# Kernel optimization log

Measured on AMD Instinct MI355X. Metric: run time of the kernel, lower is better.

The kernel has to match this reference:

```python
import jax, jax.numpy as jnp
import numpy as np

KERNEL = 3  # 2*half_size + 1 with half_size=1
ITER = 20


def _pool(v):
    # MaxPool2d(kernel=3, stride=1, padding=1) == SAME max reduce_window on NCHW
    return jax.lax.reduce_window(v, -jnp.inf, jax.lax.max,
                                 (1, 1, KERNEL, KERNEL), (1, 1, 1, 1), 'SAME')


def _erode(v):
    return -_pool(-v)


def setup_inputs() -> dict:
    key = jax.random.key(0)
    x = jax.random.normal(key, (16, 1, 1024, 1024), dtype=jnp.float32)
    return {"x": x}


def reference(x):
    skel0 = x - _pool(_erode(x))  # open(x) = dilate(erode(x))

    def step(carry, _):
        xc, skel = carry
        xc = _erode(xc)
        skel = skel + (xc - _pool(_erode(xc)))
        return (xc, skel), None

    (_, skel), _ = jax.lax.scan(step, (x, skel0), None, length=ITER)
    return skel
```

## Files before the change

kernel.cpp:

```cpp
#include <hip/hip_runtime.h>


static constexpr int W = 1024, H = 1024, NIMG = 16;
static constexpr int RCH = 32;
static constexpr int NSTEP = RCH + 16;
static constexpr int WPB = 4;
static constexpr float BIG = 3.0e38f;

__device__ __forceinline__ float min3f(float a, float b, float c) { return fminf(fminf(a, b), c); }
__device__ __forceinline__ float max3f(float a, float b, float c) { return fmaxf(fmaxf(a, b), c); }

__device__ __forceinline__ float dpp_left(float v) {
    return __int_as_float(__builtin_amdgcn_mov_dpp(__float_as_int(v), 0x138, 0xF, 0xF, true));
}
__device__ __forceinline__ float dpp_right(float v) {
    return __int_as_float(__builtin_amdgcn_mov_dpp(__float_as_int(v), 0x130, 0xF, 0xF, true));
}

template<bool FIRST, bool WRITE_E, bool EDGE, bool LE, bool RE, int SOFF>
__device__ __forceinline__
void pipe_step(int t, int y0, int gx,
               bool leftEdge, bool rightEdge, bool lane_ok,
               const float* __restrict__ in, float* __restrict__ eo,
               float* __restrict__ sk,
               float4 (&OB)[7], float4 (&MB)[7], float4& OD, float4& MD,
               float4 (&acc)[8], float4 (&pf)[2], float4 (&skpf)[2])
{
    constexpr int PFI = SOFF;

    float4 cur;
    if (!EDGE || (unsigned)t < (unsigned)H) cur = pf[PFI];
    else                                    cur = make_float4(BIG, BIG, BIG, BIG);
    {
        const int nr = t + 2;
        if ((!EDGE || (unsigned)nr < (unsigned)H) && nr <= y0 + RCH + 7)
            pf[PFI] = *(const float4*)&in[(size_t)nr * W + gx];
    }

#pragma unroll
    for (int s = 0; s < 7; ++s) {
        const float4 fOld = OB[s];
        const float4 fMid = MB[s];

        float4 vm;
        vm.x = min3f(fOld.x, fMid.x, cur.x);
        vm.y = min3f(fOld.y, fMid.y, cur.y);
        vm.z = min3f(fOld.z, fMid.z, cur.z);
        vm.w = min3f(fOld.w, fMid.w, cur.w);
        float lft = dpp_left(vm.w);
        float rgt = dpp_right(vm.x);
        if (LE && leftEdge)  lft = BIG;
        if (RE && rightEdge) rgt = BIG;
        float4 en;
        en.x = min3f(lft,  vm.x, vm.y);
        en.y = min3f(vm.x, vm.y, vm.z);
        en.z = min3f(vm.y, vm.z, vm.w);
        en.w = min3f(vm.z, vm.w, rgt);

        OB[s] = cur;

        float4 gOld, gMid;
        if (s < 6) { gOld = OB[s + 1]; gMid = MB[s + 1]; }
        else       { gOld = OD;        gMid = MD;        }
        const bool topOK = !EDGE || ((t - s - 3) >= 0);
        const bool botOK = !EDGE || ((t - s - 1) < H);
        float4 vx;
        {
            float txx = topOK ? gOld.x : -BIG, bxx = botOK ? en.x : -BIG;
            float txy = topOK ? gOld.y : -BIG, bxy = botOK ? en.y : -BIG;
            float txz = topOK ? gOld.z : -BIG, bxz = botOK ? en.z : -BIG;
            float txw = topOK ? gOld.w : -BIG, bxw = botOK ? en.w : -BIG;
            vx.x = max3f(txx, gMid.x, bxx);
            vx.y = max3f(txy, gMid.y, bxy);
            vx.z = max3f(txz, gMid.z, bxz);
            vx.w = max3f(txw, gMid.w, bxw);
        }
        float dl = dpp_left(vx.w);
        float dr = dpp_right(vx.x);
        if (LE && leftEdge)  dl = -BIG;
        if (RE && rightEdge) dr = -BIG;
        float4 dn;
        dn.x = max3f(dl,   vx.x, vx.y);
        dn.y = max3f(vx.x, vx.y, vx.z);
        dn.z = max3f(vx.y, vx.z, vx.w);
        dn.w = max3f(vx.z, vx.w, dr);

        constexpr int base = SOFF + 6;
        const int slot = base - s;
        if (s == 0) {
            acc[slot].x = fOld.x - dn.x;
            acc[slot].y = fOld.y - dn.y;
            acc[slot].z = fOld.z - dn.z;
            acc[slot].w = fOld.w - dn.w;
        } else {
            acc[slot].x += fOld.x - dn.x;
            acc[slot].y += fOld.y - dn.y;
            acc[slot].z += fOld.z - dn.z;
            acc[slot].w += fOld.w - dn.w;
        }

        if (s == 6) {
            if (WRITE_E) {
                const int er = t - 7;
                if (er >= y0 && er < y0 + RCH && lane_ok)
                    *(float4*)&eo[(size_t)er * W + gx] = en;
            }
            OD = en;
        }
        cur = en;
    }

    if (t >= y0 + 8) {
        const int r = t - 8;
        float4 v = acc[SOFF];
        if (!FIRST) {
            const float4 o = skpf[PFI];
            v.x += o.x; v.y += o.y; v.z += o.z; v.w += o.w;
        }
        if (lane_ok)
            *(float4*)&sk[(size_t)r * W + gx] = v;
    }

    if (!FIRST) {
        const int pr = t - 6;
        if (pr >= y0 && pr < y0 + RCH)
            skpf[PFI] = *(const float4*)&sk[(size_t)pr * W + gx];
    }
}

template<bool FIRST, bool WRITE_E, bool EDGE, bool LE, bool RE>
__device__ __forceinline__
void sweep(int y0, int gx,
           bool leftEdge, bool rightEdge, bool lane_ok,
           const float* __restrict__ in, float* __restrict__ eo,
           float* __restrict__ sk)
{
    float4 B0[7], B1[7], D0, D1, acc[8], pf[2], skpf[2];
    const float4 big4 = make_float4(BIG, BIG, BIG, BIG);
    const float4 z4   = make_float4(0.f, 0.f, 0.f, 0.f);
#pragma unroll
    for (int s = 0; s < 7; ++s) { B0[s] = big4; B1[s] = big4; }
    D0 = big4; D1 = big4;
#pragma unroll
    for (int j = 0; j < 8; ++j) acc[j] = z4;
    pf[0] = big4; pf[1] = big4; skpf[0] = z4; skpf[1] = z4;

    {
        const int r0 = y0 - 8, r1 = y0 - 7;
        if (!EDGE || r0 >= 0) pf[0] = *(const float4*)&in[(size_t)r0 * W + gx];
        if (!EDGE || r1 >= 0) pf[1] = *(const float4*)&in[(size_t)r1 * W + gx];
    }

    const int t0 = y0 - 8;
#pragma unroll 1
    for (int t = t0; t < t0 + NSTEP; t += 2) {
        pipe_step<FIRST, WRITE_E, EDGE, LE, RE, 0>(t,     y0, gx, leftEdge, rightEdge, lane_ok,
                                                   in, eo, sk, B0, B1, D0, D1, acc, pf, skpf);
        pipe_step<FIRST, WRITE_E, EDGE, LE, RE, 1>(t + 1, y0, gx, leftEdge, rightEdge, lane_ok,
                                                   in, eo, sk, B1, B0, D1, D0, acc, pf, skpf);
#pragma unroll
        for (int j = 0; j < 6; ++j) acc[j] = acc[j + 2];
    }
}

template<bool FIRST, bool WRITE_E>
__global__ __launch_bounds__(WPB * 64)
void skel_pipe(const float* __restrict__ ein, float* __restrict__ eout,
               float* __restrict__ skel)
{
    const int lane = threadIdx.x;
    const int bx = blockIdx.x;
    const int y0 = (blockIdx.y * WPB + (int)threadIdx.y) * RCH;
    const int img = blockIdx.z;
    const int x0 = (bx == 4) ? 768 : bx * 240;
    const int gx = x0 + 4 * lane;

    const size_t base = (size_t)img * (size_t)(W * H);
    const float* __restrict__ in = ein + base;
    float* __restrict__ eo = eout + base;
    float* __restrict__ sk = skel + base;

    const bool leftEdge  = (gx == 0);
    const bool rightEdge = (gx + 4 == W);
    const int own_lo = (bx == 0) ? 0 : ((bx == 4) ? 968 : x0 + 8);
    const int own_hi = (bx == 4) ? W : x0 + 248;
    const bool lane_ok = (gx >= own_lo) && (gx < own_hi);

    const bool edge_chunk = !(y0 >= 32 && y0 <= H - RCH - 32);

    if (bx == 0) {
        if (edge_chunk) sweep<FIRST, WRITE_E, true,  true,  false>(y0, gx, leftEdge, rightEdge, lane_ok, in, eo, sk);
        else            sweep<FIRST, WRITE_E, false, true,  false>(y0, gx, leftEdge, rightEdge, lane_ok, in, eo, sk);
    } else if (bx == 4) {
        if (edge_chunk) sweep<FIRST, WRITE_E, true,  false, true >(y0, gx, leftEdge, rightEdge, lane_ok, in, eo, sk);
        else            sweep<FIRST, WRITE_E, false, false, true >(y0, gx, leftEdge, rightEdge, lane_ok, in, eo, sk);
    } else {
        if (edge_chunk) sweep<FIRST, WRITE_E, true,  false, false>(y0, gx, leftEdge, rightEdge, lane_ok, in, eo, sk);
        else            sweep<FIRST, WRITE_E, false, false, false>(y0, gx, leftEdge, rightEdge, lane_ok, in, eo, sk);
    }
}

extern "C" void kernel_launch(void* const* d_in, const int* in_sizes, int n_in,
                              void* d_out, int out_size, void* d_ws, size_t ws_size,
                              hipStream_t stream)
{
    const float* x = (const float*)d_in[0];
    float* skel = (float*)d_out;
    const size_t n = (size_t)NIMG * W * H;

    float* e0 = (float*)d_ws;
    float* e1 = e0 + n;

    dim3 grid(5, H / (RCH * WPB), NIMG);
    dim3 block(64, WPB);

    skel_pipe<true,  true ><<<grid, block, 0, stream>>>(x,  e0, skel);
    skel_pipe<false, true ><<<grid, block, 0, stream>>>(e0, e1, skel);
    skel_pipe<false, false><<<grid, block, 0, stream>>>(e1, e0, skel);
}
```

Measured before the change: 337.2 us.

## Process two rows per pipeline step sharing vertical min/max windows

Merges the two per-row pipeline steps into one step that computes a pair of output rows together, sharing the middle-row loads between both vertical 3-tap min/max windows. This cuts redundant register moves and recomputation across the seven erosion/opening stages. It also seeds the accumulators with the prior skeleton values, loaded ahead of time, instead of keeping a separate prefetch buffer, and drops the edge-mask selects on interior chunks. The trade-off is more live registers per step, which may lower occupancy or cause spills.

```diff
diff --git a/kernel.cpp b/kernel.cpp
--- a/kernel.cpp
+++ b/kernel.cpp
@@ -17,24 +17,26 @@
     return __int_as_float(__builtin_amdgcn_mov_dpp(__float_as_int(v), 0x130, 0xF, 0xF, true));
 }
 
-template<bool FIRST, bool WRITE_E, bool EDGE, bool LE, bool RE, int SOFF>
+template<bool FIRST, bool WRITE_E, bool EDGE, bool LE, bool RE>
 __device__ __forceinline__
-void pipe_step(int t, int y0, int gx,
-               bool leftEdge, bool rightEdge, bool lane_ok,
-               const float* __restrict__ in, float* __restrict__ eo,
-               float* __restrict__ sk,
-               float4 (&OB)[7], float4 (&MB)[7], float4& OD, float4& MD,
-               float4 (&acc)[8], float4 (&pf)[2], float4 (&skpf)[2])
-{
-    constexpr int PFI = SOFF;
-
-    float4 cur;
-    if (!EDGE || (unsigned)t < (unsigned)H) cur = pf[PFI];
-    else                                    cur = make_float4(BIG, BIG, BIG, BIG);
+void pipe_step2(int t, int y0, int gx,
+                bool leftEdge, bool rightEdge, bool lane_ok,
+                const float* __restrict__ in, float* __restrict__ eo,
+                float* __restrict__ sk,
+                float4 (&OB)[7], float4 (&MB)[7], float4& OD, float4& MD,
+                float4 (&acc)[8], float4 (&pf)[2])
+{
+    float4 cur0, cur1;
+    if (!EDGE || (unsigned)t < (unsigned)H)       cur0 = pf[0];
+    else                                          cur0 = make_float4(BIG, BIG, BIG, BIG);
+    if (!EDGE || (unsigned)(t + 1) < (unsigned)H) cur1 = pf[1];
+    else                                          cur1 = make_float4(BIG, BIG, BIG, BIG);
     {
-        const int nr = t + 2;
-        if ((!EDGE || (unsigned)nr < (unsigned)H) && nr <= y0 + RCH + 7)
-            pf[PFI] = *(const float4*)&in[(size_t)nr * W + gx];
+        const int n0 = t + 2, n1 = t + 3;
+        if ((!EDGE || (unsigned)n0 < (unsigned)H) && n0 <= y0 + RCH + 7)
+            pf[0] = *(const float4*)&in[(size_t)n0 * W + gx];
+        if ((!EDGE || (unsigned)n1 < (unsigned)H) && n1 <= y0 + RCH + 7)
+            pf[1] = *(const float4*)&in[(size_t)n1 * W + gx];
     }
 
 #pragma unroll
@@ -42,89 +44,111 @@
         const float4 fOld = OB[s];
         const float4 fMid = MB[s];
 
-        float4 vm;
-        vm.x = min3f(fOld.x, fMid.x, cur.x);
-        vm.y = min3f(fOld.y, fMid.y, cur.y);
-        vm.z = min3f(fOld.z, fMid.z, cur.z);
-        vm.w = min3f(fOld.w, fMid.w, cur.w);
-        float lft = dpp_left(vm.w);
-        float rgt = dpp_right(vm.x);
-        if (LE && leftEdge)  lft = BIG;
-        if (RE && rightEdge) rgt = BIG;
-        float4 en;
-        en.x = min3f(lft,  vm.x, vm.y);
-        en.y = min3f(vm.x, vm.y, vm.z);
-        en.z = min3f(vm.y, vm.z, vm.w);
-        en.w = min3f(vm.z, vm.w, rgt);
-
-        OB[s] = cur;
+        float4 vm0, vm1;
+        vm0.x = min3f(fOld.x, fMid.x, cur0.x);
+        vm0.y = min3f(fOld.y, fMid.y, cur0.y);
+        vm0.z = min3f(fOld.z, fMid.z, cur0.z);
+        vm0.w = min3f(fOld.w, fMid.w, cur0.w);
+        vm1.x = min3f(fMid.x, cur0.x, cur1.x);
+        vm1.y = min3f(fMid.y, cur0.y, cur1.y);
+        vm1.z = min3f(fMid.z, cur0.z, cur1.z);
+        vm1.w = min3f(fMid.w, cur0.w, cur1.w);
+        float l0 = dpp_left(vm0.w), r0 = dpp_right(vm0.x);
+        float l1 = dpp_left(vm1.w), r1 = dpp_right(vm1.x);
+        if (LE && leftEdge)  { l0 = BIG; l1 = BIG; }
+        if (RE && rightEdge) { r0 = BIG; r1 = BIG; }
+        float4 en0, en1;
+        en0.x = min3f(l0,    vm0.x, vm0.y);
+        en0.y = min3f(vm0.x, vm0.y, vm0.z);
+        en0.z = min3f(vm0.y, vm0.z, vm0.w);
+        en0.w = min3f(vm0.z, vm0.w, r0);
+        en1.x = min3f(l1,    vm1.x, vm1.y);
+        en1.y = min3f(vm1.x, vm1.y, vm1.z);
+        en1.z = min3f(vm1.y, vm1.z, vm1.w);
+        en1.w = min3f(vm1.z, vm1.w, r1);
 
         float4 gOld, gMid;
         if (s < 6) { gOld = OB[s + 1]; gMid = MB[s + 1]; }
         else       { gOld = OD;        gMid = MD;        }
-        const bool topOK = !EDGE || ((t - s - 3) >= 0);
-        const bool botOK = !EDGE || ((t - s - 1) < H);
-        float4 vx;
-        {
-            float txx = topOK ? gOld.x : -BIG, bxx = botOK ? en.x : -BIG;
-            float txy = topOK ? gOld.y : -BIG, bxy = botOK ? en.y : -BIG;
-            float txz = topOK ? gOld.z : -BIG, bxz = botOK ? en.z : -BIG;
-            float txw = topOK ? gOld.w : -BIG, bxw = botOK ? en.w : -BIG;
-            vx.x = max3f(txx, gMid.x, bxx);
-            vx.y = max3f(txy, gMid.y, bxy);
-            vx.z = max3f(txz, gMid.z, bxz);
-            vx.w = max3f(txw, gMid.w, bxw);
-        }
-        float dl = dpp_left(vx.w);
-        float dr = dpp_right(vx.x);
-        if (LE && leftEdge)  dl = -BIG;
-        if (RE && rightEdge) dr = -BIG;
-        float4 dn;
-        dn.x = max3f(dl,   vx.x, vx.y);
-        dn.y = max3f(vx.x, vx.y, vx.z);
-        dn.z = max3f(vx.y, vx.z, vx.w);
-        dn.w = max3f(vx.z, vx.w, dr);
-
-        constexpr int base = SOFF + 6;
-        const int slot = base - s;
-        if (s == 0) {
-            acc[slot].x = fOld.x - dn.x;
-            acc[slot].y = fOld.y - dn.y;
-            acc[slot].z = fOld.z - dn.z;
-            acc[slot].w = fOld.w - dn.w;
+        float4 vx0, vx1;
+        if (!EDGE) {
+            vx0.x = max3f(gOld.x, gMid.x, en0.x);
+            vx0.y = max3f(gOld.y, gMid.y, en0.y);
+            vx0.z = max3f(gOld.z, gMid.z, en0.z);
+            vx0.w = max3f(gOld.w, gMid.w, en0.w);
+            vx1.x = max3f(gMid.x, en0.x, en1.x);
+            vx1.y = max3f(gMid.y, en0.y, en1.y);
+            vx1.z = max3f(gMid.z, en0.z, en1.z);
+            vx1.w = max3f(gMid.w, en0.w, en1.w);
         } else {
-            acc[slot].x += fOld.x - dn.x;
-            acc[slot].y += fOld.y - dn.y;
-            acc[slot].z += fOld.z - dn.z;
-            acc[slot].w += fOld.w - dn.w;
-        }
+            const bool topOK0 = (t - s - 3) >= 0, botOK0 = (t - s - 1) < H;
+            const bool topOK1 = (t - s - 2) >= 0, botOK1 = (t - s) < H;
+            vx0.x = max3f(topOK0 ? gOld.x : -BIG, gMid.x, botOK0 ? en0.x : -BIG);
+            vx0.y = max3f(topOK0 ? gOld.y : -BIG, gMid.y, botOK0 ? en0.y : -BIG);
+            vx0.z = max3f(topOK0 ? gOld.z : -BIG, gMid.z, botOK0 ? en0.z : -BIG);
+            vx0.w = max3f(topOK0 ? gOld.w : -BIG, gMid.w, botOK0 ? en0.w : -BIG);
+            vx1.x = max3f(topOK1 ? gMid.x : -BIG, en0.x, botOK1 ? en1.x : -BIG);
+            vx1.y = max3f(topOK1 ? gMid.y : -BIG, en0.y, botOK1 ? en1.y : -BIG);
+            vx1.z = max3f(topOK1 ? gMid.z : -BIG, en0.z, botOK1 ? en1.z : -BIG);
+            vx1.w = max3f(topOK1 ? gMid.w : -BIG, en0.w, botOK1 ? en1.w : -BIG);
+        }
+        float dl0 = dpp_left(vx0.w), dr0 = dpp_right(vx0.x);
+        float dl1 = dpp_left(vx1.w), dr1 = dpp_right(vx1.x);
+        if (LE && leftEdge)  { dl0 = -BIG; dl1 = -BIG; }
+        if (RE && rightEdge) { dr0 = -BIG; dr1 = -BIG; }
+        float4 dn0, dn1;
+        dn0.x = max3f(dl0,   vx0.x, vx0.y);
+        dn0.y = max3f(vx0.x, vx0.y, vx0.z);
+        dn0.z = max3f(vx0.y, vx0.z, vx0.w);
+        dn0.w = max3f(vx0.z, vx0.w, dr0);
+        dn1.x = max3f(dl1,   vx1.x, vx1.y);
+        dn1.y = max3f(vx1.x, vx1.y, vx1.z);
+        dn1.z = max3f(vx1.y, vx1.z, vx1.w);
+        dn1.w = max3f(vx1.z, vx1.w, dr1);
+
+        if (FIRST && s == 0) {
+            acc[6].x = fOld.x - dn0.x;  acc[6].y = fOld.y - dn0.y;
+            acc[6].z = fOld.z - dn0.z;  acc[6].w = fOld.w - dn0.w;
+            acc[7].x = fMid.x - dn1.x;  acc[7].y = fMid.y - dn1.y;
+            acc[7].z = fMid.z - dn1.z;  acc[7].w = fMid.w - dn1.w;
+        } else {
+            acc[6 - s].x += fOld.x - dn0.x;  acc[6 - s].y += fOld.y - dn0.y;
+            acc[6 - s].z += fOld.z - dn0.z;  acc[6 - s].w += fOld.w - dn0.w;
+            acc[7 - s].x += fMid.x - dn1.x;  acc[7 - s].y += fMid.y - dn1.y;
+            acc[7 - s].z += fMid.z - dn1.z;  acc[7 - s].w += fMid.w - dn1.w;
+        }
+
+        OB[s] = cur0;
+        MB[s] = cur1;
 
         if (s == 6) {
             if (WRITE_E) {
-                const int er = t - 7;
-                if (er >= y0 && er < y0 + RCH && lane_ok)
-                    *(float4*)&eo[(size_t)er * W + gx] = en;
+                const int er0 = t - 7, er1 = t - 6;
+                if (er0 >= y0 && er0 < y0 + RCH && lane_ok)
+                    *(float4*)&eo[(size_t)er0 * W + gx] = en0;
+                if (er1 >= y0 && er1 < y0 + RCH && lane_ok)
+                    *(float4*)&eo[(size_t)er1 * W + gx] = en1;
             }
-            OD = en;
-        }
-        cur = en;
+            OD = en0;
+            MD = en1;
+        }
+        cur0 = en0;
+        cur1 = en1;
     }
 
     if (t >= y0 + 8) {
-        const int r = t - 8;
-        float4 v = acc[SOFF];
-        if (!FIRST) {
-            const float4 o = skpf[PFI];
-            v.x += o.x; v.y += o.y; v.z += o.z; v.w += o.w;
-        }
-        if (lane_ok)
-            *(float4*)&sk[(size_t)r * W + gx] = v;
-    }
-
+        if (lane_ok) {
+            *(float4*)&sk[(size_t)(t - 8) * W + gx] = acc[0];
+            *(float4*)&sk[(size_t)(t - 7) * W + gx] = acc[1];
+        }
+    }
+#pragma unroll
+    for (int j = 0; j < 6; ++j) acc[j] = acc[j + 2];
     if (!FIRST) {
-        const int pr = t - 6;
-        if (pr >= y0 && pr < y0 + RCH)
-            skpf[PFI] = *(const float4*)&sk[(size_t)pr * W + gx];
+        if (t >= y0 && t < y0 + RCH)
+            acc[6] = *(const float4*)&sk[(size_t)t * W + gx];
+        if (t + 1 >= y0 && t + 1 < y0 + RCH)
+            acc[7] = *(const float4*)&sk[(size_t)(t + 1) * W + gx];
     }
 }
 
@@ -135,15 +159,15 @@
            const float* __restrict__ in, float* __restrict__ eo,
            float* __restrict__ sk)
 {
-    float4 B0[7], B1[7], D0, D1, acc[8], pf[2], skpf[2];
+    float4 OB[7], MB[7], OD, MD, acc[8], pf[2];
     const float4 big4 = make_float4(BIG, BIG, BIG, BIG);
     const float4 z4   = make_float4(0.f, 0.f, 0.f, 0.f);
 #pragma unroll
-    for (int s = 0; s < 7; ++s) { B0[s] = big4; B1[s] = big4; }
-    D0 = big4; D1 = big4;
+    for (int s = 0; s < 7; ++s) { OB[s] = big4; MB[s] = big4; }
+    OD = big4; MD = big4;
 #pragma unroll
     for (int j = 0; j < 8; ++j) acc[j] = z4;
-    pf[0] = big4; pf[1] = big4; skpf[0] = z4; skpf[1] = z4;
+    pf[0] = big4; pf[1] = big4;
 
     {
         const int r0 = y0 - 8, r1 = y0 - 7;
@@ -154,12 +178,8 @@
     const int t0 = y0 - 8;
 #pragma unroll 1
     for (int t = t0; t < t0 + NSTEP; t += 2) {
-        pipe_step<FIRST, WRITE_E, EDGE, LE, RE, 0>(t,     y0, gx, leftEdge, rightEdge, lane_ok,
-                                                   in, eo, sk, B0, B1, D0, D1, acc, pf, skpf);
-        pipe_step<FIRST, WRITE_E, EDGE, LE, RE, 1>(t + 1, y0, gx, leftEdge, rightEdge, lane_ok,
-                                                   in, eo, sk, B1, B0, D1, D0, acc, pf, skpf);
-#pragma unroll
-        for (int j = 0; j < 6; ++j) acc[j] = acc[j + 2];
+        pipe_step2<FIRST, WRITE_E, EDGE, LE, RE>(t, y0, gx, leftEdge, rightEdge, lane_ok,
+                                                 in, eo, sk, OB, MB, OD, MD, acc, pf);
     }
 }
 
```

Result: faster. 326.9 us (-3.0%).
